# Kernel tuning notes

Hardware: AMD Instinct MI355X
Metric: run time of the kernel (lower is better)

Reference implementation:

```python
import jax, jax.numpy as jnp
import numpy as np

# Soft decision tree: heap-ordered full binary tree.
# Inner node n (0-based heap index) has gate p_n = sigmoid(beta_n * (x @ W_n + b_n)).
# Children of n are 2n+1 (left, prob 1-p) and 2n+2 (right, prob p).

LMBDA = 0.1


def setup_inputs() -> dict:
    key = jax.random.key(0)
    k = jax.random.split(key, 6)
    B, IN, OUT, D = 8192, 2048, 100, 8
    N = 2 ** D - 1          # inner nodes = 255
    L = 2 ** D              # leaves = 256
    x = jax.random.normal(k[0], (B, IN), dtype=jnp.float32)
    labels = jax.random.randint(k[1], (B,), 0, OUT, dtype=jnp.int32)
    W = jax.random.normal(k[2], (N, IN), dtype=jnp.float32) * 0.02
    b = jax.random.normal(k[3], (N,), dtype=jnp.float32) * 0.02
    beta = jax.random.normal(k[4], (N,), dtype=jnp.float32)
    leaf_params = jax.random.normal(k[5], (L, OUT), dtype=jnp.float32)
    return {"x": x, "labels": labels, "W": W, "b": b, "beta": beta,
            "leaf_params": leaf_params}


def _tree_paths(p, depth):
    """p: [B, N] gate probs in heap order. Returns (inner_path [B,N], leaf_path [B,L])."""
    B = p.shape[0]
    path = jnp.ones((B, 1), p.dtype)
    inner_paths = []
    start = 0
    for d in range(depth):
        width = 2 ** d
        p_lvl = p[:, start:start + width]          # [B, width]
        inner_paths.append(path)                   # path prob arriving at each inner node
        left = path * (1.0 - p_lvl)
        right = path * p_lvl
        # interleave -> heap order of next level: [l0, r0, l1, r1, ...]
        path = jnp.stack([left, right], axis=-1).reshape(B, 2 * width)
        start += width
    return jnp.concatenate(inner_paths, axis=1), path


def reference(x, labels, W, b, beta, leaf_params):
    N = W.shape[0]
    D = int(np.log2(N + 1))            # max_depth
    OUT = leaf_params.shape[1]

    # All inner-node gates in one GEMM: sigmoid(beta * (x @ W^T + b))
    p = jax.nn.sigmoid(beta[None, :] * (x @ W.T + b[None, :]))   # [B, N]
    inner_path, leaf_path = _tree_paths(p, D)                    # [B,N], [B,L]

    # Leaf distributions: softmax over each leaf's params
    logQ = jax.nn.log_softmax(leaf_params, axis=-1)              # [L, OUT]
    Q = jnp.exp(logQ)                                            # [L, OUT]

    # y one-hot; TQ[b, l] = y_b . log Q_l
    y = jax.nn.one_hot(labels, OUT, dtype=x.dtype)               # [B, OUT]
    TQ = y @ logQ.T                                              # [B, L]
    loss = jnp.mean(jnp.sum(leaf_path * TQ, axis=1))
    neg_loss = -loss

    # Penalty: only inner nodes whose children are also inner (depth 1..D-1)
    n_pen = 2 ** (D - 1) - 1
    alpha = jnp.sum(p * inner_path, axis=0) / jnp.sum(inner_path, axis=0)  # [N]
    node_idx = np.arange(N)
    depths = np.floor(np.log2(node_idx + 1)).astype(np.int32) + 1
    lmbda_arr = jnp.asarray(LMBDA * (2.0 ** (-depths)), dtype=x.dtype)     # [N]
    a = alpha[:n_pen]
    C = -jnp.sum(lmbda_arr[:n_pen] * 0.5 * (jnp.log(a) + jnp.log1p(-a)))

    # Output: leaf distribution of the max-path-prob leaf per sample
    best_leaf = jnp.argmax(leaf_path, axis=1)                    # [B]
    output = Q[best_leaf]                                        # [B, OUT]

    return neg_loss, output, C
```

## Files before the change

kernel.cpp:

```cpp
#include <hip/hip_runtime.h>
#include <math.h>

typedef __attribute__((ext_vector_type(4)))  short short4v;
typedef __attribute__((ext_vector_type(8)))  short short8v;
typedef __attribute__((ext_vector_type(4)))  float f32x4;

#define OFF_LOGQT 256
#define OFF_Q     25856
#define OFF_WHI   51456
#define OFF_WLO   313600
#define OFF_P0    575744
#define OFF_P1    2672896

__device__ __forceinline__ unsigned short f2bf(float f) {
    unsigned int b = __float_as_uint(f);
    unsigned int r = (b + 0x7FFFu + ((b >> 16) & 1u)) >> 16;
    return (unsigned short)r;
}
__device__ __forceinline__ float bf2f(unsigned short u) {
    return __uint_as_float(((unsigned int)u) << 16);
}

__global__ __launch_bounds__(256) void k_wconv(const float* __restrict__ W,
                                               unsigned short* __restrict__ whi,
                                               unsigned short* __restrict__ wlo)
{
    int g = (blockIdx.x * 256 + threadIdx.x) * 8;
    int row = g >> 11;
    unsigned short h[8], l[8];
    if (row < 255) {
        const float* src = W + (size_t)row * 2048 + (g & 2047);
        float4 v0 = *(const float4*)src;
        float4 v1 = *(const float4*)(src + 4);
        float vv[8] = {v0.x, v0.y, v0.z, v0.w, v1.x, v1.y, v1.z, v1.w};
#pragma unroll
        for (int j = 0; j < 8; ++j) {
            h[j] = f2bf(vv[j]);
            l[j] = f2bf(vv[j] - bf2f(h[j]));
        }
    } else {
#pragma unroll
        for (int j = 0; j < 8; ++j) { h[j] = 0; l[j] = 0; }
    }
#pragma unroll
    for (int j = 0; j < 8; ++j) { whi[g + j] = h[j]; wlo[g + j] = l[j]; }
}

__global__ __launch_bounds__(64) void k_logsoftmax(const float* __restrict__ lp,
                                                   float* __restrict__ logQT,
                                                   float* __restrict__ Q)
{
    int r = blockIdx.x;
    int lane = threadIdx.x;
    float v0 = (lane < 100)      ? lp[r * 100 + lane]      : -INFINITY;
    float v1 = (lane + 64 < 100) ? lp[r * 100 + lane + 64] : -INFINITY;
    float m = fmaxf(v0, v1);
    for (int s = 32; s; s >>= 1) m = fmaxf(m, __shfl_xor(m, s));
    float e = 0.f;
    if (lane < 100)      e += expf(v0 - m);
    if (lane + 64 < 100) e += expf(v1 - m);
    for (int s = 32; s; s >>= 1) e += __shfl_xor(e, s);
    float logZ = m + logf(e);
    if (lane < 100) {
        float lq = v0 - logZ;
        Q[r * 100 + lane] = expf(lq);
        logQT[lane * 256 + r] = lq;
    }
    if (lane + 64 < 100) {
        float lq = v1 - logZ;
        Q[r * 100 + lane + 64] = expf(lq);
        logQT[(lane + 64) * 256 + r] = lq;
    }
}

#define GBK 64
#define LDR 136

__global__ __launch_bounds__(256, 1) void k_gemm(const float* __restrict__ x,
                                                 const unsigned short* __restrict__ whi,
                                                 const unsigned short* __restrict__ wlo,
                                                 float* __restrict__ part,
                                                 int ksteps)
{
    __shared__ unsigned short As[128 * LDR];
    __shared__ unsigned short Bs[128 * LDR];

    const int tid  = threadIdx.x;
    const int w    = tid >> 6, lane = tid & 63;
    const int wm   = w >> 1, wn = w & 1;
    const int r16  = lane & 15, hi8 = (lane >> 4) * 8;
    const int row0 = blockIdx.x * 128;
    const int col0 = blockIdx.y * 128;
    const int kz   = blockIdx.z;
    const size_t kbase = (size_t)kz * ksteps * GBK;
    float* pdst = part + (size_t)kz * (8192 * 256);

    f32x4 acc[4][4] = {};

    float4  aR[8];
    short8v bH[4], bL[4];

    auto GL = [&](int s) {
        const size_t k0 = kbase + (size_t)s * GBK;
#pragma unroll
        for (int i = 0; i < 8; ++i) {
            int g = tid + i * 256;
            int ar = g >> 4, ac = (g & 15) * 4;
            aR[i] = *(const float4*)(x + (size_t)(row0 + ar) * 2048 + k0 + ac);
        }
#pragma unroll
        for (int i = 0; i < 4; ++i) {
            int g = tid + i * 256;
            int br = g >> 3, bc = (g & 7) * 8;
            size_t wo = (size_t)(col0 + br) * 2048 + k0 + bc;
            bH[i] = *(const short8v*)(whi + wo);
            bL[i] = *(const short8v*)(wlo + wo);
        }
    };

    auto DSW = [&]() {
#pragma unroll
        for (int i = 0; i < 8; ++i) {
            int g = tid + i * 256;
            int ar = g >> 4, ac = (g & 15) * 4;
            float vv[4] = {aR[i].x, aR[i].y, aR[i].z, aR[i].w};
            short4v hv, lv;
#pragma unroll
            for (int j = 0; j < 4; ++j) {
                unsigned short hb = f2bf(vv[j]);
                hv[j] = (short)hb;
                lv[j] = (short)f2bf(vv[j] - bf2f(hb));
            }
            *(short4v*)&As[ar * LDR + ac]      = hv;
            *(short4v*)&As[ar * LDR + 64 + ac] = lv;
        }
#pragma unroll
        for (int i = 0; i < 4; ++i) {
            int g = tid + i * 256;
            int br = g >> 3, bc = (g & 7) * 8;
            *(short8v*)&Bs[br * LDR + bc]      = bH[i];
            *(short8v*)&Bs[br * LDR + 64 + bc] = bL[i];
        }
    };

    GL(0);
    for (int s = 0; s < ksteps; ++s) {
        DSW();
        __syncthreads();
        if (s + 1 < ksteps) GL(s + 1);
#pragma unroll
        for (int kk = 0; kk < 2; ++kk) {
            const int kc = kk * 32 + hi8;
            short8v ah[4], al[4];
#pragma unroll
            for (int fm = 0; fm < 4; ++fm) {
                int base = (wm * 64 + fm * 16 + r16) * LDR + kc;
                ah[fm] = *(const short8v*)&As[base];
                al[fm] = *(const short8v*)&As[base + 64];
            }
#pragma unroll
            for (int fn = 0; fn < 4; ++fn) {
                int bb = (wn * 64 + fn * 16 + r16) * LDR + kc;
                short8v bhh = *(const short8v*)&Bs[bb];
                short8v bll = *(const short8v*)&Bs[bb + 64];
#pragma unroll
                for (int fm = 0; fm < 4; ++fm) {
                    acc[fm][fn] = __builtin_amdgcn_mfma_f32_16x16x32_bf16(ah[fm], bhh, acc[fm][fn], 0, 0, 0);
                    acc[fm][fn] = __builtin_amdgcn_mfma_f32_16x16x32_bf16(ah[fm], bll, acc[fm][fn], 0, 0, 0);
                    acc[fm][fn] = __builtin_amdgcn_mfma_f32_16x16x32_bf16(al[fm], bhh, acc[fm][fn], 0, 0, 0);
                }
            }
        }
        __syncthreads();
    }

#pragma unroll
    for (int fm = 0; fm < 4; ++fm) {
#pragma unroll
        for (int fn = 0; fn < 4; ++fn) {
            int col = col0 + wn * 64 + fn * 16 + r16;
#pragma unroll
            for (int j = 0; j < 4; ++j) {
                int row = row0 + wm * 64 + fm * 16 + (lane >> 4) * 4 + j;
                pdst[(size_t)row * 256 + col] = acc[fm][fn][j];
            }
        }
    }
}

__global__ __launch_bounds__(256) void k_sig(float* __restrict__ p0,
                                             const float* __restrict__ p1,
                                             const float* __restrict__ bias,
                                             const float* __restrict__ beta,
                                             int use2)
{
    int idx = blockIdx.x * 256 + threadIdx.x;
    float4 a = ((const float4*)p0)[idx];
    float4 b = use2 ? ((const float4*)p1)[idx] : make_float4(0.f, 0.f, 0.f, 0.f);
    int c0 = (idx & 63) * 4;
    float av[4] = {a.x, a.y, a.z, a.w};
    float bv[4] = {b.x, b.y, b.z, b.w};
    float r[4];
#pragma unroll
    for (int j = 0; j < 4; ++j) {
        int c = c0 + j; if (c > 254) c = 254;
        float t = beta[c] * (av[j] + bv[j] + bias[c]);
        r[j] = 1.f / (1.f + expf(-t));
    }
    ((float4*)p0)[idx] = make_float4(r[0], r[1], r[2], r[3]);
}

__global__ __launch_bounds__(256) void k_tree(const float* __restrict__ p,
                                              const int* __restrict__ labels,
                                              const float* __restrict__ logQT,
                                              const float* __restrict__ Q,
                                              float* __restrict__ accum,
                                              float* __restrict__ out)
{
    __shared__ float psh[4][256];
    __shared__ float accPI[127];
    __shared__ float accI[127];
    __shared__ float loss_sh;
    int tid = threadIdx.x;
    int w = tid >> 6, lane = tid & 63;
    if (tid < 127) { accPI[tid] = 0.f; accI[tid] = 0.f; }
    if (tid == 255) loss_sh = 0.f;
    __syncthreads();

    for (int rr = 0; rr < 2; ++rr) {
        int b = blockIdx.x * 8 + w * 2 + rr;
        *(float4*)&psh[w][lane * 4] = *(const float4*)&p[(size_t)b * 256 + lane * 4];
        asm volatile("s_waitcnt lgkmcnt(0)" ::: "memory");
        __builtin_amdgcn_sched_barrier(0);

        int label = labels[b];
        float4 tq = *(const float4*)&logQT[(size_t)label * 256 + lane * 4];

        float prefix = 1.f;
#pragma unroll
        for (int d = 0; d < 6; ++d) {
            int node = (1 << d) - 1 + (lane >> (6 - d));
            float g = psh[w][node];
            prefix *= ((lane >> (5 - d)) & 1) ? g : (1.f - g);
        }
        float g6  = psh[w][63 + lane];
        float p60 = prefix * (1.f - g6), p61 = prefix * g6;
        float g7a = psh[w][127 + 2 * lane];
        float g7b = psh[w][128 + 2 * lane];
        float f0 = p60 * (1.f - g7a), f1 = p60 * g7a;
        float f2 = p61 * (1.f - g7b), f3 = p61 * g7b;

        float lsum = f0 * tq.x + f1 * tq.y + f2 * tq.z + f3 * tq.w;

        float best = f0; int bestIdx = lane * 4;
        if (f1 > best) { best = f1; bestIdx = lane * 4 + 1; }
        if (f2 > best) { best = f2; bestIdx = lane * 4 + 2; }
        if (f3 > best) { best = f3; bestIdx = lane * 4 + 3; }

        for (int s = 32; s; s >>= 1) lsum += __shfl_xor(lsum, s);
        for (int s = 32; s; s >>= 1) {
            float ov = __shfl_xor(best, s);
            int   oi = __shfl_xor(bestIdx, s);
            if (ov > best || (ov == best && oi < bestIdx)) { best = ov; bestIdx = oi; }
        }
        if (lane == 0) atomicAdd(&loss_sh, lsum);

#pragma unroll
        for (int t = 0; t < 2; ++t) {
            int n = lane + t * 64;
            if (n < 127) {
                float f = 1.f;
                int cur = n;
                while (cur > 0) {
                    int par = (cur - 1) >> 1;
                    float g = psh[w][par];
                    f *= (cur == 2 * par + 2) ? g : (1.f - g);
                    cur = par;
                }
                atomicAdd(&accPI[n], psh[w][n] * f);
                atomicAdd(&accI[n], f);
            }
        }

        const float* qrow = Q + (size_t)bestIdx * 100;
        float* orow = out + 1 + (size_t)b * 100;
        orow[lane] = qrow[lane];
        if (lane < 36) orow[64 + lane] = qrow[64 + lane];
    }

    __syncthreads();
    if (tid < 127) {
        atomicAdd(&accum[1 + tid],   accPI[tid]);
        atomicAdd(&accum[128 + tid], accI[tid]);
    }
    if (tid == 0) atomicAdd(&accum[0], loss_sh);
}

__global__ __launch_bounds__(128) void k_final(const float* __restrict__ accum,
                                               float* __restrict__ out)
{
    __shared__ float s[128];
    int t = threadIdx.x;
    float term = 0.f;
    if (t < 127) {
        float a = accum[1 + t] / accum[128 + t];
        int depth = 32 - __clz(t + 1);
        float lmbda = 0.1f * exp2f(-(float)depth);
        term = -lmbda * 0.5f * (logf(a) + log1pf(-a));
    }
    s[t] = term;
    __syncthreads();
    if (t == 0) {
        float c = 0.f;
        for (int i = 0; i < 127; ++i) c += s[i];
        out[819201] = c;
        out[0] = -accum[0] / 8192.0f;
    }
}

extern "C" void kernel_launch(void* const* d_in, const int* in_sizes, int n_in,
                              void* d_out, int out_size, void* d_ws, size_t ws_size,
                              hipStream_t stream)
{
    const float* x      = (const float*)d_in[0];
    const int*   labels = (const int*)  d_in[1];
    const float* W      = (const float*)d_in[2];
    const float* bias   = (const float*)d_in[3];
    const float* beta   = (const float*)d_in[4];
    const float* leaf   = (const float*)d_in[5];
    float* out = (float*)d_out;
    float* ws  = (float*)d_ws;

    float*          accum = ws;
    float*          logQT = ws + OFF_LOGQT;
    float*          Q     = ws + OFF_Q;
    unsigned short* whi   = (unsigned short*)(ws + OFF_WHI);
    unsigned short* wlo   = (unsigned short*)(ws + OFF_WLO);
    float*          part0 = ws + OFF_P0;
    float*          part1 = ws + OFF_P1;

    const size_t need2 = (size_t)(OFF_P1 + 8192 * 256) * sizeof(float);
    const int use2 = (ws_size >= need2) ? 1 : 0;
    const int ksteps = use2 ? 16 : 32;

    hipMemsetAsync(accum, 0, 256 * sizeof(float), stream);
    k_wconv<<<256, 256, 0, stream>>>(W, whi, wlo);
    k_logsoftmax<<<256, 64, 0, stream>>>(leaf, logQT, Q);
    k_gemm<<<dim3(64, 2, use2 ? 2 : 1), 256, 0, stream>>>(x, whi, wlo, part0, ksteps);
    k_sig<<<2048, 256, 0, stream>>>(part0, part1, bias, beta, use2);
    k_tree<<<1024, 256, 0, stream>>>(part0, labels, logQT, Q, accum, out);
    k_final<<<1, 128, 0, stream>>>(accum, out);
}
```

Measured before the change: 201.6 us.

## Fuse sigmoid into tree kernel, merge prep kernels, raise split-K to four

The separate sigmoid pass is removed: the tree kernel now sums the split-K partials and applies bias, beta and sigmoid itself. The weight conversion, leaf log-softmax and accumulator zeroing are merged into one prep kernel, which also replaces the memset. Shared-memory atomics in the tree kernel become per-lane register accumulators followed by a cross-wave reduction. Split-K can now go to 4 when the workspace allows, giving the GEMM 512 blocks instead of 256 but requiring more partial-sum traffic to be read back in the tree kernel.

```diff
diff --git a/kernel.cpp b/kernel.cpp
--- a/kernel.cpp
+++ b/kernel.cpp
@@ -10,7 +10,7 @@
 #define OFF_WHI   51456
 #define OFF_WLO   313600
 #define OFF_P0    575744
-#define OFF_P1    2672896
+#define PART_STRIDE 2097152
 
 __device__ __forceinline__ unsigned short f2bf(float f) {
     unsigned int b = __float_as_uint(f);
@@ -21,55 +21,58 @@
     return __uint_as_float(((unsigned int)u) << 16);
 }
 
-__global__ __launch_bounds__(256) void k_wconv(const float* __restrict__ W,
-                                               unsigned short* __restrict__ whi,
-                                               unsigned short* __restrict__ wlo)
-{
-    int g = (blockIdx.x * 256 + threadIdx.x) * 8;
-    int row = g >> 11;
-    unsigned short h[8], l[8];
-    if (row < 255) {
-        const float* src = W + (size_t)row * 2048 + (g & 2047);
-        float4 v0 = *(const float4*)src;
-        float4 v1 = *(const float4*)(src + 4);
-        float vv[8] = {v0.x, v0.y, v0.z, v0.w, v1.x, v1.y, v1.z, v1.w};
-#pragma unroll
-        for (int j = 0; j < 8; ++j) {
-            h[j] = f2bf(vv[j]);
-            l[j] = f2bf(vv[j] - bf2f(h[j]));
-        }
+__global__ __launch_bounds__(256) void k_prep(const float* __restrict__ W,
+                                              unsigned short* __restrict__ whi,
+                                              unsigned short* __restrict__ wlo,
+                                              const float* __restrict__ lp,
+                                              float* __restrict__ logQT,
+                                              float* __restrict__ Q,
+                                              float* __restrict__ accum)
+{
+    const int bx = blockIdx.x, tid = threadIdx.x;
+    if (bx < 256) {
+        if (bx == 0) accum[tid] = 0.f;
+        int g = (bx * 256 + tid) * 8;
+        int row = g >> 11;
+        unsigned short h[8], l[8];
+        if (row < 255) {
+            const float* src = W + (size_t)row * 2048 + (g & 2047);
+            float4 v0 = *(const float4*)src;
+            float4 v1 = *(const float4*)(src + 4);
+            float vv[8] = {v0.x, v0.y, v0.z, v0.w, v1.x, v1.y, v1.z, v1.w};
+#pragma unroll
+            for (int j = 0; j < 8; ++j) {
+                h[j] = f2bf(vv[j]);
+                l[j] = f2bf(vv[j] - bf2f(h[j]));
+            }
+        } else {
+#pragma unroll
+            for (int j = 0; j < 8; ++j) { h[j] = 0; l[j] = 0; }
+        }
+#pragma unroll
+        for (int j = 0; j < 8; ++j) { whi[g + j] = h[j]; wlo[g + j] = l[j]; }
     } else {
-#pragma unroll
-        for (int j = 0; j < 8; ++j) { h[j] = 0; l[j] = 0; }
-    }
-#pragma unroll
-    for (int j = 0; j < 8; ++j) { whi[g + j] = h[j]; wlo[g + j] = l[j]; }
-}
-
-__global__ __launch_bounds__(64) void k_logsoftmax(const float* __restrict__ lp,
-                                                   float* __restrict__ logQT,
-                                                   float* __restrict__ Q)
-{
-    int r = blockIdx.x;
-    int lane = threadIdx.x;
-    float v0 = (lane < 100)      ? lp[r * 100 + lane]      : -INFINITY;
-    float v1 = (lane + 64 < 100) ? lp[r * 100 + lane + 64] : -INFINITY;
-    float m = fmaxf(v0, v1);
-    for (int s = 32; s; s >>= 1) m = fmaxf(m, __shfl_xor(m, s));
-    float e = 0.f;
-    if (lane < 100)      e += expf(v0 - m);
-    if (lane + 64 < 100) e += expf(v1 - m);
-    for (int s = 32; s; s >>= 1) e += __shfl_xor(e, s);
-    float logZ = m + logf(e);
-    if (lane < 100) {
-        float lq = v0 - logZ;
-        Q[r * 100 + lane] = expf(lq);
-        logQT[lane * 256 + r] = lq;
-    }
-    if (lane + 64 < 100) {
-        float lq = v1 - logZ;
-        Q[r * 100 + lane + 64] = expf(lq);
-        logQT[(lane + 64) * 256 + r] = lq;
+        int w = tid >> 6, lane = tid & 63;
+        int r = (bx - 256) * 4 + w;
+        float v0 = (lane < 100)      ? lp[r * 100 + lane]      : -INFINITY;
+        float v1 = (lane + 64 < 100) ? lp[r * 100 + lane + 64] : -INFINITY;
+        float m = fmaxf(v0, v1);
+        for (int s = 32; s; s >>= 1) m = fmaxf(m, __shfl_xor(m, s));
+        float e = 0.f;
+        if (lane < 100)      e += expf(v0 - m);
+        if (lane + 64 < 100) e += expf(v1 - m);
+        for (int s = 32; s; s >>= 1) e += __shfl_xor(e, s);
+        float logZ = m + logf(e);
+        if (lane < 100) {
+            float lq = v0 - logZ;
+            Q[r * 100 + lane] = expf(lq);
+            logQT[lane * 256 + r] = lq;
+        }
+        if (lane + 64 < 100) {
+            float lq = v1 - logZ;
+            Q[r * 100 + lane + 64] = expf(lq);
+            logQT[(lane + 64) * 256 + r] = lq;
+        }
     }
 }
 
@@ -93,7 +96,7 @@
     const int col0 = blockIdx.y * 128;
     const int kz   = blockIdx.z;
     const size_t kbase = (size_t)kz * ksteps * GBK;
-    float* pdst = part + (size_t)kz * (8192 * 256);
+    float* pdst = part + (size_t)kz * PART_STRIDE;
 
     f32x4 acc[4][4] = {};
 
@@ -188,29 +191,9 @@
     }
 }
 
-__global__ __launch_bounds__(256) void k_sig(float* __restrict__ p0,
-                                             const float* __restrict__ p1,
-                                             const float* __restrict__ bias,
-                                             const float* __restrict__ beta,
-                                             int use2)
-{
-    int idx = blockIdx.x * 256 + threadIdx.x;
-    float4 a = ((const float4*)p0)[idx];
-    float4 b = use2 ? ((const float4*)p1)[idx] : make_float4(0.f, 0.f, 0.f, 0.f);
-    int c0 = (idx & 63) * 4;
-    float av[4] = {a.x, a.y, a.z, a.w};
-    float bv[4] = {b.x, b.y, b.z, b.w};
-    float r[4];
-#pragma unroll
-    for (int j = 0; j < 4; ++j) {
-        int c = c0 + j; if (c > 254) c = 254;
-        float t = beta[c] * (av[j] + bv[j] + bias[c]);
-        r[j] = 1.f / (1.f + expf(-t));
-    }
-    ((float4*)p0)[idx] = make_float4(r[0], r[1], r[2], r[3]);
-}
-
-__global__ __launch_bounds__(256) void k_tree(const float* __restrict__ p,
+__global__ __launch_bounds__(256) void k_tree(const float* __restrict__ part, int npart,
+                                              const float* __restrict__ bias,
+                                              const float* __restrict__ beta,
                                               const int* __restrict__ labels,
                                               const float* __restrict__ logQT,
                                               const float* __restrict__ Q,
@@ -218,23 +201,43 @@
                                               float* __restrict__ out)
 {
     __shared__ float psh[4][256];
-    __shared__ float accPI[127];
-    __shared__ float accI[127];
-    __shared__ float loss_sh;
-    int tid = threadIdx.x;
-    int w = tid >> 6, lane = tid & 63;
-    if (tid < 127) { accPI[tid] = 0.f; accI[tid] = 0.f; }
-    if (tid == 255) loss_sh = 0.f;
-    __syncthreads();
+    __shared__ float redPI[4][128];
+    __shared__ float redI[4][128];
+    __shared__ float lossw[4];
+    const int tid = threadIdx.x;
+    const int w = tid >> 6, lane = tid & 63;
+    const int c0 = lane * 4;
+
+    float4 bi, be;
+    if (lane < 63) {
+        bi = *(const float4*)&bias[c0];
+        be = *(const float4*)&beta[c0];
+    } else {
+        bi = make_float4(bias[252], bias[253], bias[254], 0.f);
+        be = make_float4(beta[252], beta[253], beta[254], 0.f);
+    }
+
+    float aPI0 = 0.f, aPI1 = 0.f, aI0 = 0.f, aI1 = 0.f, lossAcc = 0.f;
 
     for (int rr = 0; rr < 2; ++rr) {
         int b = blockIdx.x * 8 + w * 2 + rr;
-        *(float4*)&psh[w][lane * 4] = *(const float4*)&p[(size_t)b * 256 + lane * 4];
+
+        float4 s = make_float4(0.f, 0.f, 0.f, 0.f);
+        for (int z = 0; z < npart; ++z) {
+            float4 v = *(const float4*)&part[(size_t)z * PART_STRIDE + (size_t)b * 256 + c0];
+            s.x += v.x; s.y += v.y; s.z += v.z; s.w += v.w;
+        }
+        float4 pv;
+        pv.x = 1.f / (1.f + expf(-be.x * (s.x + bi.x)));
+        pv.y = 1.f / (1.f + expf(-be.y * (s.y + bi.y)));
+        pv.z = 1.f / (1.f + expf(-be.z * (s.z + bi.z)));
+        pv.w = 1.f / (1.f + expf(-be.w * (s.w + bi.w)));
+        *(float4*)&psh[w][c0] = pv;
         asm volatile("s_waitcnt lgkmcnt(0)" ::: "memory");
         __builtin_amdgcn_sched_barrier(0);
 
         int label = labels[b];
-        float4 tq = *(const float4*)&logQT[(size_t)label * 256 + lane * 4];
+        float4 tq = *(const float4*)&logQT[(size_t)label * 256 + c0];
 
         float prefix = 1.f;
 #pragma unroll
@@ -252,34 +255,44 @@
 
         float lsum = f0 * tq.x + f1 * tq.y + f2 * tq.z + f3 * tq.w;
 
-        float best = f0; int bestIdx = lane * 4;
-        if (f1 > best) { best = f1; bestIdx = lane * 4 + 1; }
-        if (f2 > best) { best = f2; bestIdx = lane * 4 + 2; }
-        if (f3 > best) { best = f3; bestIdx = lane * 4 + 3; }
-
-        for (int s = 32; s; s >>= 1) lsum += __shfl_xor(lsum, s);
-        for (int s = 32; s; s >>= 1) {
-            float ov = __shfl_xor(best, s);
-            int   oi = __shfl_xor(bestIdx, s);
+        float best = f0; int bestIdx = c0;
+        if (f1 > best) { best = f1; bestIdx = c0 + 1; }
+        if (f2 > best) { best = f2; bestIdx = c0 + 2; }
+        if (f3 > best) { best = f3; bestIdx = c0 + 3; }
+
+        for (int sft = 32; sft; sft >>= 1) lsum += __shfl_xor(lsum, sft);
+        for (int sft = 32; sft; sft >>= 1) {
+            float ov = __shfl_xor(best, sft);
+            int   oi = __shfl_xor(bestIdx, sft);
             if (ov > best || (ov == best && oi < bestIdx)) { best = ov; bestIdx = oi; }
         }
-        if (lane == 0) atomicAdd(&loss_sh, lsum);
-
-#pragma unroll
-        for (int t = 0; t < 2; ++t) {
-            int n = lane + t * 64;
-            if (n < 127) {
-                float f = 1.f;
-                int cur = n;
-                while (cur > 0) {
-                    int par = (cur - 1) >> 1;
-                    float g = psh[w][par];
-                    f *= (cur == 2 * par + 2) ? g : (1.f - g);
-                    cur = par;
-                }
-                atomicAdd(&accPI[n], psh[w][n] * f);
-                atomicAdd(&accI[n], f);
-            }
+        lossAcc += lsum;
+
+        {
+            int n = lane;
+            float f = 1.f;
+            int cur = n;
+            while (cur > 0) {
+                int par = (cur - 1) >> 1;
+                float g = psh[w][par];
+                f *= (cur == 2 * par + 2) ? g : (1.f - g);
+                cur = par;
+            }
+            aPI0 += psh[w][n] * f;
+            aI0  += f;
+        }
+        if (lane < 63) {
+            int n = lane + 64;
+            float f = 1.f;
+            int cur = n;
+            while (cur > 0) {
+                int par = (cur - 1) >> 1;
+                float g = psh[w][par];
+                f *= (cur == 2 * par + 2) ? g : (1.f - g);
+                cur = par;
+            }
+            aPI1 += psh[w][n] * f;
+            aI1  += f;
         }
 
         const float* qrow = Q + (size_t)bestIdx * 100;
@@ -288,12 +301,20 @@
         if (lane < 36) orow[64 + lane] = qrow[64 + lane];
     }
 
+    redPI[w][lane] = aPI0;           redI[w][lane] = aI0;
+    redPI[w][64 + lane] = (lane < 63) ? aPI1 : 0.f;
+    redI [w][64 + lane] = (lane < 63) ? aI1  : 0.f;
+    if (lane == 0) lossw[w] = lossAcc;
     __syncthreads();
     if (tid < 127) {
-        atomicAdd(&accum[1 + tid],   accPI[tid]);
-        atomicAdd(&accum[128 + tid], accI[tid]);
-    }
-    if (tid == 0) atomicAdd(&accum[0], loss_sh);
+        float sPI = redPI[0][tid] + redPI[1][tid] + redPI[2][tid] + redPI[3][tid];
+        float sI  = redI [0][tid] + redI [1][tid] + redI [2][tid] + redI [3][tid];
+        atomicAdd(&accum[1 + tid],   sPI);
+        atomicAdd(&accum[128 + tid], sI);
+    }
+    if (tid == 128) {
+        atomicAdd(&accum[0], lossw[0] + lossw[1] + lossw[2] + lossw[3]);
+    }
 }
 
 __global__ __launch_bounds__(128) void k_final(const float* __restrict__ accum,
@@ -336,18 +357,16 @@
     float*          Q     = ws + OFF_Q;
     unsigned short* whi   = (unsigned short*)(ws + OFF_WHI);
     unsigned short* wlo   = (unsigned short*)(ws + OFF_WLO);
-    float*          part0 = ws + OFF_P0;
-    float*          part1 = ws + OFF_P1;
-
-    const size_t need2 = (size_t)(OFF_P1 + 8192 * 256) * sizeof(float);
-    const int use2 = (ws_size >= need2) ? 1 : 0;
-    const int ksteps = use2 ? 16 : 32;
-
-    hipMemsetAsync(accum, 0, 256 * sizeof(float), stream);
-    k_wconv<<<256, 256, 0, stream>>>(W, whi, wlo);
-    k_logsoftmax<<<256, 64, 0, stream>>>(leaf, logQT, Q);
-    k_gemm<<<dim3(64, 2, use2 ? 2 : 1), 256, 0, stream>>>(x, whi, wlo, part0, ksteps);
-    k_sig<<<2048, 256, 0, stream>>>(part0, part1, bias, beta, use2);
-    k_tree<<<1024, 256, 0, stream>>>(part0, labels, logQT, Q, accum, out);
+    float*          part  = ws + OFF_P0;
+
+    auto need = [](int k) {
+        return (size_t)(OFF_P0 + (size_t)k * PART_STRIDE) * sizeof(float);
+    };
+    int ksplit = (ws_size >= need(4)) ? 4 : (ws_size >= need(2)) ? 2 : 1;
+    int ksteps = 32 / ksplit;
+
+    k_prep<<<320, 256, 0, stream>>>(W, whi, wlo, leaf, logQT, Q, accum);
+    k_gemm<<<dim3(64, 2, ksplit), 256, 0, stream>>>(x, whi, wlo, part, ksteps);
+    k_tree<<<1024, 256, 0, stream>>>(part, ksplit, bias, beta, labels, logQT, Q, accum, out);
     k_final<<<1, 128, 0, stream>>>(accum, out);
 }
```

Result: faster. 194.0 us (-3.8%).
